# Optimization experiments

Hardware: AMD Instinct MI355X
Metric: run time of the kernel (lower is better)

## Reference

```python
import jax, jax.numpy as jnp
import numpy as np

B, SQ, SK, D_MODEL, H, D = 2, 2048, 2048, 1024, 16, 64


def setup_inputs() -> dict:
    key = jax.random.key(0)
    ks = jax.random.split(key, 10)
    s = 1.0 / np.sqrt(D_MODEL)
    return {
        "x": jax.random.normal(ks[0], (B, SK, D_MODEL), jnp.float32),
        "x2": jax.random.normal(ks[1], (B, SQ, D_MODEL), jnp.float32),
        "Wq": jax.random.normal(ks[2], (H, D_MODEL, D), jnp.float32) * s,
        "bq": jax.random.normal(ks[3], (H, D), jnp.float32) * s,
        "Wk": jax.random.normal(ks[4], (H, D_MODEL, D), jnp.float32) * s,
        "bk": jax.random.normal(ks[5], (H, D), jnp.float32) * s,
        "Wv": jax.random.normal(ks[6], (H, D_MODEL, D), jnp.float32) * s,
        "bv": jax.random.normal(ks[7], (H, D), jnp.float32) * s,
        "Wo": jax.random.normal(ks[8], (D_MODEL, D_MODEL), jnp.float32) * s,
        "bo": jax.random.normal(ks[9], (D_MODEL,), jnp.float32) * s,
    }


def reference(x, x2, Wq, bq, Wk, bk, Wv, bv, Wo, bo):
    # Batched per-head projections (fuses the Python per-head loop).
    # q: [B, H, SQ, D]; k,v: [B, H, SK, D]
    q = jnp.einsum("bsm,hmd->bhsd", x2, Wq) + bq[None, :, None, :]
    k = jnp.einsum("bsm,hmd->bhsd", x, Wk) + bk[None, :, None, :]
    v = jnp.einsum("bsm,hmd->bhsd", x, Wv) + bv[None, :, None, :]
    scale = 1.0 / jnp.sqrt(jnp.asarray(D, q.dtype))
    scores = jnp.einsum("bhqd,bhkd->bhqk", q, k) * scale  # [B,H,SQ,SK]
    attn = jax.nn.softmax(scores, axis=-1)
    o = jnp.einsum("bhqk,bhkd->bhqd", attn, v)  # [B,H,SQ,D]
    # concat heads along feature dim (head-major order matches torch.cat)
    o = o.transpose(0, 2, 1, 3).reshape(B, SQ, H * D)
    # final projection; dropout is identity in eval mode
    return o @ Wo.T + bo
```

## Files before the change

### kernel.cpp

```cpp
#include <hip/hip_runtime.h>
#include <math.h>

#define B_   2
#define SQ_  2048
#define SK_  2048
#define DM_  1024
#define H_   16
#define D_   64

typedef __attribute__((ext_vector_type(8))) short bf16x8;
typedef __attribute__((ext_vector_type(4))) float f32x4;
typedef unsigned int u32;

__device__ __forceinline__ short f2bf(float f) {
    union { float f; unsigned u; } v; v.f = f;
    unsigned r = v.u + 0x7FFFu + ((v.u >> 16) & 1u);
    return (short)(r >> 16);
}
__device__ __forceinline__ u32 pk2bf(float x, float y) {
    union { float f; u32 u; } a, b; a.f = x; b.f = y;
    return ((a.u + 0x8000u) >> 16) | ((b.u + 0x8000u) & 0xFFFF0000u);
}
__device__ __forceinline__ u32 pkbf_rh(float x, float y) {
    union { float f; u32 u; } a, b; a.f = x; b.f = y;
    return __builtin_amdgcn_perm(b.u + 0x8000u, a.u + 0x8000u, 0x07060302u);
}

__device__ __forceinline__ void gll16(const void* g, void* l) {
    __builtin_amdgcn_global_load_lds(
        (const __attribute__((address_space(1))) u32*)g,
        (__attribute__((address_space(3))) u32*)l, 16, 0, 0);
}

__global__ __launch_bounds__(256) void prep_kernel(
    const float* __restrict__ Wq, const float* __restrict__ Wk,
    const float* __restrict__ Wv, const float* __restrict__ Wo,
    const float* __restrict__ x,  const float* __restrict__ x2,
    short* __restrict__ WqT, short* __restrict__ WkT,
    short* __restrict__ WvT, short* __restrict__ Wob,
    short* __restrict__ xb,  short* __restrict__ x2b)
{
    const int t = threadIdx.x;
    const int z = blockIdx.z;
    if (z >= 3) {
        const float* src = (z == 3) ? Wo : (z == 4) ? x : x2;
        short* dst       = (z == 3) ? Wob : (z == 4) ? xb : x2b;
        int nloop = (z == 3) ? 4 : 16;
        int bid = blockIdx.y * 16 + blockIdx.x;
        #pragma unroll 4
        for (int j = 0; j < nloop; j++) {
            int i = bid * (nloop * 256) + j * 256 + t;
            float4 v = ((const float4*)src)[i];
            short4 s;
            s.x = f2bf(v.x); s.y = f2bf(v.y); s.z = f2bf(v.z); s.w = f2bf(v.w);
            ((short4*)dst)[i] = s;
        }
        return;
    }
    const float* W = (z == 0) ? Wq : (z == 1) ? Wk : Wv;
    short* WT      = (z == 0) ? WqT : (z == 1) ? WkT : WvT;
    const int h  = blockIdx.y;
    const int m0 = blockIdx.x * 64;
    __shared__ short Ls[64][68];

    #pragma unroll
    for (int it = 0; it < 4; it++) {
        int lin = it * 256 + t;
        int m = lin >> 4, d4 = lin & 15;
        float4 v = *(const float4*)&W[((long)h * DM_ + m0 + m) * D_ + d4 * 4];
        short4 s;
        s.x = f2bf(v.x); s.y = f2bf(v.y); s.z = f2bf(v.z); s.w = f2bf(v.w);
        *(short4*)&Ls[m][d4 * 4] = s;
    }
    __syncthreads();
    #pragma unroll
    for (int it = 0; it < 2; it++) {
        int d = (t >> 3) + it * 32, scol = t & 7;
        bf16x8 vv;
        #pragma unroll
        for (int j = 0; j < 8; j++) vv[j] = Ls[scol * 8 + j][d];
        *(bf16x8*)&WT[((long)h * 64 + d) * DM_ + m0 + scol * 8] = vv;
    }
}

template <int MODE>
__device__ __forceinline__ void gemm_core(
    const short* __restrict__ A, const short* __restrict__ Bw,
    const float* __restrict__ bias, void* __restrict__ outp,
    int r0, int n0, float oscale)
{
    __shared__ short As[128 * 64];
    __shared__ short Bs[128 * 64];

    const int t    = threadIdx.x;
    const int w    = t >> 6;
    const int ln   = t & 63;
    const int l15  = ln & 15;
    const int quad = ln >> 4;
    const int wr   = w >> 1;
    const int wc   = w & 1;

    f32x4 acc[4][4];
    #pragma unroll
    for (int i = 0; i < 4; i++)
        #pragma unroll
        for (int j = 0; j < 4; j++) acc[i][j] = (f32x4){0.f, 0.f, 0.f, 0.f};

    const int srow = ln >> 3;
    const int sc   = (ln & 7) ^ srow;
    const int rsw  = l15 & 7;

    for (int k0 = 0; k0 < 1024; k0 += 64) {
        __syncthreads();
        #pragma unroll
        for (int j = 0; j < 4; j++) {
            int q   = w * 4 + j;
            int row = q * 8 + srow;
            gll16(A  + ((long)(r0 + row) << 10) + k0 + sc * 8, As + q * 512);
            gll16(Bw + ((long)(n0 + row) << 10) + k0 + sc * 8, Bs + q * 512);
        }
        __syncthreads();
        #pragma unroll
        for (int kh = 0; kh < 2; kh++) {
            bf16x8 af[4], bfr[4];
            #pragma unroll
            for (int i = 0; i < 4; i++) {
                int ra = wr * 64 + i * 16 + l15;
                int rb = wc * 64 + i * 16 + l15;
                int pc = ((kh * 4 + quad) ^ rsw) * 8;
                af[i]  = *(const bf16x8*)&As[ra * 64 + pc];
                bfr[i] = *(const bf16x8*)&Bs[rb * 64 + pc];
            }
            #pragma unroll
            for (int i = 0; i < 4; i++)
                #pragma unroll
                for (int j = 0; j < 4; j++)
                    acc[i][j] = __builtin_amdgcn_mfma_f32_16x16x32_bf16(
                        af[i], bfr[j], acc[i][j], 0, 0, 0);
        }
    }

    #pragma unroll
    for (int j = 0; j < 4; j++) {
        int col = n0 + wc * 64 + j * 16 + l15;
        float bv = bias[col];
        if (MODE == 2) {
            int hh = col >> 6, dd = col & 63;
            #pragma unroll
            for (int i = 0; i < 4; i++) {
                int rowb = r0 + wr * 64 + i * 16 + quad * 4;
                int bb = rowb >> 11, ss = rowb & 2047;
                int sl = ss & 63;
                int sp = (ss & ~63) | (sl & 35) | ((sl & 12) << 1) | ((sl & 16) >> 2);
                short4 sv;
                sv.x = f2bf(acc[i][j][0] + bv);
                sv.y = f2bf(acc[i][j][1] + bv);
                sv.z = f2bf(acc[i][j][2] + bv);
                sv.w = f2bf(acc[i][j][3] + bv);
                *(short4*)&((short*)outp)[
                    ((long)(((bb << 4) + hh) * 64 + dd) << 11) + sp] = sv;
            }
        } else {
            #pragma unroll
            for (int i = 0; i < 4; i++) {
                int rowb = r0 + wr * 64 + i * 16 + quad * 4;
                #pragma unroll
                for (int r = 0; r < 4; r++) {
                    float v = (acc[i][j][r] + bv) * oscale;
                    if (MODE == 0)
                        ((short*)outp)[(long)(rowb + r) * 1024 + col] = f2bf(v);
                    else
                        ((float*)outp)[(long)(rowb + r) * 1024 + col] = v;
                }
            }
        }
    }
}

#define QSCALE 0.180336880977f

__global__ __launch_bounds__(256) void gemm_qkv_kernel(
    const short* __restrict__ x2b, const short* __restrict__ xb,
    const short* __restrict__ WqT, const short* __restrict__ WkT,
    const short* __restrict__ WvT,
    const float* __restrict__ bq, const float* __restrict__ bk,
    const float* __restrict__ bv,
    short* __restrict__ Qb, short* __restrict__ Kb, short* __restrict__ VT)
{
    const int z = blockIdx.z;
    if (z == 0) {
        gemm_core<0>(x2b, WqT, bq, Qb, blockIdx.x * 128, blockIdx.y * 128, QSCALE);
    } else if (z == 1) {
        gemm_core<0>(xb, WkT, bk, Kb, blockIdx.x * 128, blockIdx.y * 128, 1.0f);
    } else {
        gemm_core<2>(xb, WvT, bv, VT, blockIdx.x * 128, blockIdx.y * 128, 1.0f);
    }
}

__global__ __launch_bounds__(256) void gemm_out_kernel(
    const short* __restrict__ A, const short* __restrict__ Bw,
    const float* __restrict__ bias, float* __restrict__ outp)
{
    __shared__ short As[64 * 64];
    __shared__ short Bs[128 * 64];

    const int r0   = blockIdx.x * 64;
    const int n0   = blockIdx.y * 128;
    const int t    = threadIdx.x;
    const int w    = t >> 6;
    const int ln   = t & 63;
    const int l15  = ln & 15;
    const int quad = ln >> 4;
    const int wr   = w >> 1;
    const int wc   = w & 1;

    f32x4 acc[2][4];
    #pragma unroll
    for (int i = 0; i < 2; i++)
        #pragma unroll
        for (int j = 0; j < 4; j++) acc[i][j] = (f32x4){0.f, 0.f, 0.f, 0.f};

    const int srow = ln >> 3;
    const int sc   = (ln & 7) ^ srow;
    const int rsw  = l15 & 7;

    for (int k0 = 0; k0 < 1024; k0 += 64) {
        __syncthreads();
        #pragma unroll
        for (int j = 0; j < 6; j++) {
            int q = w * 6 + j;
            if (q < 8) {
                int row = q * 8 + srow;
                gll16(A + ((long)(r0 + row) << 10) + k0 + sc * 8, As + q * 512);
            } else {
                int qb = q - 8;
                int row = qb * 8 + srow;
                gll16(Bw + ((long)(n0 + row) << 10) + k0 + sc * 8, Bs + qb * 512);
            }
        }
        __syncthreads();
        #pragma unroll
        for (int kh = 0; kh < 2; kh++) {
            int pc = ((kh * 4 + quad) ^ rsw) * 8;
            bf16x8 af[2], bfr[4];
            #pragma unroll
            for (int i = 0; i < 2; i++)
                af[i] = *(const bf16x8*)&As[(wr * 32 + i * 16 + l15) * 64 + pc];
            #pragma unroll
            for (int j = 0; j < 4; j++)
                bfr[j] = *(const bf16x8*)&Bs[(wc * 64 + j * 16 + l15) * 64 + pc];
            #pragma unroll
            for (int i = 0; i < 2; i++)
                #pragma unroll
                for (int j = 0; j < 4; j++)
                    acc[i][j] = __builtin_amdgcn_mfma_f32_16x16x32_bf16(
                        af[i], bfr[j], acc[i][j], 0, 0, 0);
        }
    }

    #pragma unroll
    for (int j = 0; j < 4; j++) {
        int col = n0 + wc * 64 + j * 16 + l15;
        float bv = bias[col];
        #pragma unroll
        for (int i = 0; i < 2; i++) {
            int rowb = r0 + wr * 32 + i * 16 + quad * 4;
            #pragma unroll
            for (int r = 0; r < 4; r++)
                outp[(long)(rowb + r) * 1024 + col] = acc[i][j][r] + bv;
        }
    }
}

__global__ __launch_bounds__(256, 2) void flash_kernel(
    const short* __restrict__ Q, const short* __restrict__ K,
    const short* __restrict__ VT, short* __restrict__ O)
{
    const int t    = threadIdx.x;
    const int wave = t >> 6;
    const int ln   = t & 63;
    const int l15  = ln & 15;
    const int quad = ln >> 4;
    const int bh = blockIdx.y;
    const int b  = bh >> 4;
    const int h  = bh & 15;
    const int q0 = blockIdx.x * 128;
    const int wq = q0 + wave * 32;

    __shared__ short Ks[2][2][64 * 64];
    __shared__ short Vs[2][2][64 * 64];

    const int srow = ln >> 3;
    const int sc   = (ln & 7) ^ srow;
    const int rsw  = l15 & 7;
    const int pc0  = ((quad    ) ^ rsw) * 8;
    const int pc1  = ((quad + 4) ^ rsw) * 8;
    const int rb   = l15 * 64;

    bf16x8 aQ0[2], aQ1[2];
    #pragma unroll
    for (int qg = 0; qg < 2; qg++) {
        const short* Qp = Q + ((long)(b * SQ_ + wq + qg * 16 + l15)) * 1024
                            + h * 64 + quad * 8;
        aQ0[qg] = *(const bf16x8*)(Qp);
        aQ1[qg] = *(const bf16x8*)(Qp + 32);
    }

    bf16x8 ones;
    #pragma unroll
    for (int j = 0; j < 8; j++) ones[j] = (short)0x3F80;

    const f32x4 fz = (f32x4){0.f, 0.f, 0.f, 0.f};

    f32x4 o_acc[2][4];
    f32x4 l_acc[2];
    #pragma unroll
    for (int qg = 0; qg < 2; qg++) {
        l_acc[qg] = fz;
        #pragma unroll
        for (int i = 0; i < 4; i++) o_acc[qg][i] = fz;
    }

    const short* Kbase = K  + ((long)b * SK_) * 1024 + h * 64;
    const short* Vbase = VT + (long)bh * D_ * SK_;
    const int qqa = wave * 2, qqb = wave * 2 + 1;
    const int rowa = qqa * 8 + srow, rowb_ = qqb * 8 + srow;

    #define STAGE(bufp, half, kbase)                                            \
        gll16(Kbase + (long)((kbase) + rowa)  * 1024 + sc * 8,                  \
              &Ks[bufp][half][qqa * 512]);                                      \
        gll16(Kbase + (long)((kbase) + rowb_) * 1024 + sc * 8,                  \
              &Ks[bufp][half][qqb * 512]);                                      \
        gll16(Vbase + (long)rowa  * 2048 + (kbase) + sc * 8,                    \
              &Vs[bufp][half][qqa * 512]);                                      \
        gll16(Vbase + (long)rowb_ * 2048 + (kbase) + sc * 8,                    \
              &Vs[bufp][half][qqb * 512]);

    STAGE(0, 0, 0)
    STAGE(0, 1, 64)

    int cur = 0;
    for (int k0 = 0; k0 < SK_; k0 += 128) {
        __syncthreads();
        if (k0 + 128 < SK_) {
            int nx = cur ^ 1;
            STAGE(nx, 0, k0 + 128)
            STAGE(nx, 1, k0 + 192)
        }
        const short* K0 = &Ks[cur][0][0];
        const short* K1 = &Ks[cur][1][0];
        const short* V0 = &Vs[cur][0][0];
        const short* V1 = &Vs[cur][1][0];

        bf16x8 kfA[8];
        #pragma unroll
        for (int kt = 0; kt < 4; kt++) {
            const short* kr = &K0[kt * 1024 + rb];
            kfA[kt * 2    ] = *(const bf16x8*)&kr[pc0];
            kfA[kt * 2 + 1] = *(const bf16x8*)&kr[pc1];
        }

        bf16x8 kfB[8];
        #pragma unroll
        for (int kt = 0; kt < 4; kt++) {
            const short* kr = &K1[kt * 1024 + rb];
            kfB[kt * 2    ] = *(const bf16x8*)&kr[pc0];
            kfB[kt * 2 + 1] = *(const bf16x8*)&kr[pc1];
        }
        f32x4 zA[2][4], zB[2][4];
        #pragma unroll
        for (int kt = 0; kt < 4; kt++)
            #pragma unroll
            for (int qg = 0; qg < 2; qg++) {
                f32x4 z = __builtin_amdgcn_mfma_f32_16x16x32_bf16(kfA[kt * 2], aQ0[qg], fz, 0, 0, 0);
                zA[qg][kt] = __builtin_amdgcn_mfma_f32_16x16x32_bf16(kfA[kt * 2 + 1], aQ1[qg], z, 0, 0, 0);
            }

        bf16x8 vfA[8];
        #pragma unroll
        for (int dt = 0; dt < 4; dt++) {
            const short* vr = &V0[dt * 1024 + rb];
            vfA[dt * 2    ] = *(const bf16x8*)&vr[pc0];
            vfA[dt * 2 + 1] = *(const bf16x8*)&vr[pc1];
        }
        u32 pwA[2][8], pwB[2][8];
        #pragma unroll
        for (int kt = 0; kt < 4; kt++) {
            #pragma unroll
            for (int qg = 0; qg < 2; qg++) {
                f32x4 z = __builtin_amdgcn_mfma_f32_16x16x32_bf16(kfB[kt * 2], aQ0[qg], fz, 0, 0, 0);
                zB[qg][kt] = __builtin_amdgcn_mfma_f32_16x16x32_bf16(kfB[kt * 2 + 1], aQ1[qg], z, 0, 0, 0);
            }
            #pragma unroll
            for (int qg = 0; qg < 2; qg++) {
                f32x4 s = zA[qg][kt];
                pwA[qg][kt * 2    ] = pkbf_rh(__builtin_amdgcn_exp2f(s[0]),
                                              __builtin_amdgcn_exp2f(s[1]));
                pwA[qg][kt * 2 + 1] = pkbf_rh(__builtin_amdgcn_exp2f(s[2]),
                                              __builtin_amdgcn_exp2f(s[3]));
            }
        }

        bf16x8 aP0A[2], aP1A[2];
        #pragma unroll
        for (int qg = 0; qg < 2; qg++) {
            union { bf16x8 v; u32 w[4]; } u0, u1;
            u0.w[0] = pwA[qg][0]; u0.w[1] = pwA[qg][1];
            u0.w[2] = pwA[qg][2]; u0.w[3] = pwA[qg][3];
            u1.w[0] = pwA[qg][4]; u1.w[1] = pwA[qg][5];
            u1.w[2] = pwA[qg][6]; u1.w[3] = pwA[qg][7];
            aP0A[qg] = u0.v; aP1A[qg] = u1.v;
            l_acc[qg] = __builtin_amdgcn_mfma_f32_16x16x32_bf16(aP0A[qg], ones, l_acc[qg], 0, 0, 0);
            l_acc[qg] = __builtin_amdgcn_mfma_f32_16x16x32_bf16(aP1A[qg], ones, l_acc[qg], 0, 0, 0);
        }

        bf16x8 vfB[8];
        #pragma unroll
        for (int dt = 0; dt < 4; dt++) {
            const short* vr = &V1[dt * 1024 + rb];
            vfB[dt * 2    ] = *(const bf16x8*)&vr[pc0];
            vfB[dt * 2 + 1] = *(const bf16x8*)&vr[pc1];
        }
        #pragma unroll
        for (int dt = 0; dt < 4; dt++) {
            #pragma unroll
            for (int qg = 0; qg < 2; qg++) {
                o_acc[qg][dt] = __builtin_amdgcn_mfma_f32_16x16x32_bf16(aP0A[qg], vfA[dt * 2    ], o_acc[qg][dt], 0, 0, 0);
                o_acc[qg][dt] = __builtin_amdgcn_mfma_f32_16x16x32_bf16(aP1A[qg], vfA[dt * 2 + 1], o_acc[qg][dt], 0, 0, 0);
            }
            #pragma unroll
            for (int qg = 0; qg < 2; qg++) {
                f32x4 s = zB[qg][dt];
                pwB[qg][dt * 2    ] = pkbf_rh(__builtin_amdgcn_exp2f(s[0]),
                                              __builtin_amdgcn_exp2f(s[1]));
                pwB[qg][dt * 2 + 1] = pkbf_rh(__builtin_amdgcn_exp2f(s[2]),
                                              __builtin_amdgcn_exp2f(s[3]));
            }
        }

        bf16x8 aP0B[2], aP1B[2];
        #pragma unroll
        for (int qg = 0; qg < 2; qg++) {
            union { bf16x8 v; u32 w[4]; } u0, u1;
            u0.w[0] = pwB[qg][0]; u0.w[1] = pwB[qg][1];
            u0.w[2] = pwB[qg][2]; u0.w[3] = pwB[qg][3];
            u1.w[0] = pwB[qg][4]; u1.w[1] = pwB[qg][5];
            u1.w[2] = pwB[qg][6]; u1.w[3] = pwB[qg][7];
            aP0B[qg] = u0.v; aP1B[qg] = u1.v;
        }
        __builtin_amdgcn_s_setprio(1);
        #pragma unroll
        for (int qg = 0; qg < 2; qg++) {
            l_acc[qg] = __builtin_amdgcn_mfma_f32_16x16x32_bf16(aP0B[qg], ones, l_acc[qg], 0, 0, 0);
            l_acc[qg] = __builtin_amdgcn_mfma_f32_16x16x32_bf16(aP1B[qg], ones, l_acc[qg], 0, 0, 0);
        }
        #pragma unroll
        for (int dt = 0; dt < 4; dt++) {
            #pragma unroll
            for (int qg = 0; qg < 2; qg++) {
                o_acc[qg][dt] = __builtin_amdgcn_mfma_f32_16x16x32_bf16(aP0B[qg], vfB[dt * 2    ], o_acc[qg][dt], 0, 0, 0);
                o_acc[qg][dt] = __builtin_amdgcn_mfma_f32_16x16x32_bf16(aP1B[qg], vfB[dt * 2 + 1], o_acc[qg][dt], 0, 0, 0);
            }
        }
        __builtin_amdgcn_s_setprio(0);
        cur ^= 1;
    }
    #undef STAGE

    #pragma unroll
    for (int qg = 0; qg < 2; qg++) {
        #pragma unroll
        for (int r = 0; r < 4; r++) {
            float inv = 1.0f / l_acc[qg][r];
            long row = (long)b * SQ_ + wq + qg * 16 + quad * 4 + r;
            short* Op = O + row * 1024 + h * 64 + l15;
            #pragma unroll
            for (int dt = 0; dt < 4; dt++)
                Op[dt * 16] = f2bf(o_acc[qg][dt][r] * inv);
        }
    }
}

extern "C" void kernel_launch(void* const* d_in, const int* in_sizes, int n_in,
                              void* d_out, int out_size, void* d_ws, size_t ws_size,
                              hipStream_t stream) {
    const float* x  = (const float*)d_in[0];
    const float* x2 = (const float*)d_in[1];
    const float* Wq = (const float*)d_in[2];
    const float* bq = (const float*)d_in[3];
    const float* Wk = (const float*)d_in[4];
    const float* bk = (const float*)d_in[5];
    const float* Wv = (const float*)d_in[6];
    const float* bv = (const float*)d_in[7];
    const float* Wo = (const float*)d_in[8];
    const float* bo = (const float*)d_in[9];
    float* out = (float*)d_out;

    const size_t nAct = (size_t)B_ * SK_ * DM_;
    const size_t nW   = (size_t)DM_ * DM_;
    short* bufA = (short*)d_ws;
    short* bufB = bufA + nAct;
    short* Qb   = bufB + nAct;
    short* Kb   = Qb + nAct;
    short* VTws = Kb + nAct;
    short* WqT  = VTws + nAct;
    short* WkT  = WqT + nW;
    short* WvT  = WkT + nW;
    short* Wob  = WvT + nW;

    prep_kernel<<<dim3(16, 16, 6), 256, 0, stream>>>(
        Wq, Wk, Wv, Wo, x, x2, WqT, WkT, WvT, Wob, bufA, bufB);

    gemm_qkv_kernel<<<dim3(32, 8, 3), 256, 0, stream>>>(
        bufB, bufA, WqT, WkT, WvT, bq, bk, bv, Qb, Kb, VTws);

    flash_kernel<<<dim3(16, 32), 256, 0, stream>>>(Qb, Kb, VTws, bufB);
    gemm_out_kernel<<<dim3(64, 8), 256, 0, stream>>>(bufB, Wob, bo, out);
}
```

Measured before the change: 204.6 us.

## Double-buffer LDS tiles in QKV and output projection GEMMs

Both projection GEMMs now use two LDS buffers. Each iteration issues the async global-to-LDS loads for the next K slice before running the MFMAs on the current slice, and drops one barrier per iteration. The aim is to overlap global memory latency with matrix compute. The cost is doubled LDS use (64 KB per block in the QKV kernel), which may lower the number of resident blocks per CU.

```diff
diff --git a/kernel.cpp b/kernel.cpp
--- a/kernel.cpp
+++ b/kernel.cpp
@@ -83,15 +83,27 @@
     }
 }
 
+__device__ __forceinline__ void gemm_stage(
+    short* __restrict__ Asb, short* __restrict__ Bsb,
+    const short* __restrict__ A, const short* __restrict__ Bw,
+    int r0, int n0, int k0c, int w, int srow, int sc)
+{
+    #pragma unroll
+    for (int j = 0; j < 4; j++) {
+        int q   = w * 4 + j;
+        int row = q * 8 + srow;
+        gll16(A  + ((long)(r0 + row) << 10) + k0c + sc * 8, Asb + q * 512);
+        gll16(Bw + ((long)(n0 + row) << 10) + k0c + sc * 8, Bsb + q * 512);
+    }
+}
+
 template <int MODE>
 __device__ __forceinline__ void gemm_core(
+    short* __restrict__ Ls,
     const short* __restrict__ A, const short* __restrict__ Bw,
     const float* __restrict__ bias, void* __restrict__ outp,
     int r0, int n0, float oscale)
 {
-    __shared__ short As[128 * 64];
-    __shared__ short Bs[128 * 64];
-
     const int t    = threadIdx.x;
     const int w    = t >> 6;
     const int ln   = t & 63;
@@ -110,16 +122,17 @@
     const int sc   = (ln & 7) ^ srow;
     const int rsw  = l15 & 7;
 
+    gemm_stage(Ls, Ls + 8192, A, Bw, r0, n0, 0, w, srow, sc);
+
+    int cur = 0;
     for (int k0 = 0; k0 < 1024; k0 += 64) {
         __syncthreads();
-        #pragma unroll
-        for (int j = 0; j < 4; j++) {
-            int q   = w * 4 + j;
-            int row = q * 8 + srow;
-            gll16(A  + ((long)(r0 + row) << 10) + k0 + sc * 8, As + q * 512);
-            gll16(Bw + ((long)(n0 + row) << 10) + k0 + sc * 8, Bs + q * 512);
-        }
-        __syncthreads();
+        if (k0 + 64 < 1024) {
+            short* Anx = Ls + (cur ^ 1) * 16384;
+            gemm_stage(Anx, Anx + 8192, A, Bw, r0, n0, k0 + 64, w, srow, sc);
+        }
+        const short* Asb = Ls + cur * 16384;
+        const short* Bsb = Asb + 8192;
         #pragma unroll
         for (int kh = 0; kh < 2; kh++) {
             bf16x8 af[4], bfr[4];
@@ -128,8 +141,8 @@
                 int ra = wr * 64 + i * 16 + l15;
                 int rb = wc * 64 + i * 16 + l15;
                 int pc = ((kh * 4 + quad) ^ rsw) * 8;
-                af[i]  = *(const bf16x8*)&As[ra * 64 + pc];
-                bfr[i] = *(const bf16x8*)&Bs[rb * 64 + pc];
+                af[i]  = *(const bf16x8*)&Asb[ra * 64 + pc];
+                bfr[i] = *(const bf16x8*)&Bsb[rb * 64 + pc];
             }
             #pragma unroll
             for (int i = 0; i < 4; i++)
@@ -138,6 +151,7 @@
                     acc[i][j] = __builtin_amdgcn_mfma_f32_16x16x32_bf16(
                         af[i], bfr[j], acc[i][j], 0, 0, 0);
         }
+        cur ^= 1;
     }
 
     #pragma unroll
@@ -187,13 +201,33 @@
     const float* __restrict__ bv,
     short* __restrict__ Qb, short* __restrict__ Kb, short* __restrict__ VT)
 {
+    __shared__ short Ls[2 * 16384];
     const int z = blockIdx.z;
     if (z == 0) {
-        gemm_core<0>(x2b, WqT, bq, Qb, blockIdx.x * 128, blockIdx.y * 128, QSCALE);
+        gemm_core<0>(Ls, x2b, WqT, bq, Qb, blockIdx.x * 128, blockIdx.y * 128, QSCALE);
     } else if (z == 1) {
-        gemm_core<0>(xb, WkT, bk, Kb, blockIdx.x * 128, blockIdx.y * 128, 1.0f);
+        gemm_core<0>(Ls, xb, WkT, bk, Kb, blockIdx.x * 128, blockIdx.y * 128, 1.0f);
     } else {
-        gemm_core<2>(xb, WvT, bv, VT, blockIdx.x * 128, blockIdx.y * 128, 1.0f);
+        gemm_core<2>(Ls, xb, WvT, bv, VT, blockIdx.x * 128, blockIdx.y * 128, 1.0f);
+    }
+}
+
+__device__ __forceinline__ void gout_stage(
+    short* __restrict__ Asb, short* __restrict__ Bsb,
+    const short* __restrict__ A, const short* __restrict__ Bw,
+    int r0, int n0, int k0c, int w, int srow, int sc)
+{
+    #pragma unroll
+    for (int j = 0; j < 6; j++) {
+        int q = w * 6 + j;
+        if (q < 8) {
+            int row = q * 8 + srow;
+            gll16(A + ((long)(r0 + row) << 10) + k0c + sc * 8, Asb + q * 512);
+        } else {
+            int qb = q - 8;
+            int row = qb * 8 + srow;
+            gll16(Bw + ((long)(n0 + row) << 10) + k0c + sc * 8, Bsb + qb * 512);
+        }
     }
 }
 
@@ -201,8 +235,7 @@
     const short* __restrict__ A, const short* __restrict__ Bw,
     const float* __restrict__ bias, float* __restrict__ outp)
 {
-    __shared__ short As[64 * 64];
-    __shared__ short Bs[128 * 64];
+    __shared__ short Ls[2 * 12288];
 
     const int r0   = blockIdx.x * 64;
     const int n0   = blockIdx.y * 128;
@@ -224,31 +257,27 @@
     const int sc   = (ln & 7) ^ srow;
     const int rsw  = l15 & 7;
 
+    gout_stage(Ls, Ls + 4096, A, Bw, r0, n0, 0, w, srow, sc);
+
+    int cur = 0;
     for (int k0 = 0; k0 < 1024; k0 += 64) {
         __syncthreads();
-        #pragma unroll
-        for (int j = 0; j < 6; j++) {
-            int q = w * 6 + j;
-            if (q < 8) {
-                int row = q * 8 + srow;
-                gll16(A + ((long)(r0 + row) << 10) + k0 + sc * 8, As + q * 512);
-            } else {
-                int qb = q - 8;
-                int row = qb * 8 + srow;
-                gll16(Bw + ((long)(n0 + row) << 10) + k0 + sc * 8, Bs + qb * 512);
-            }
-        }
-        __syncthreads();
+        if (k0 + 64 < 1024) {
+            short* Anx = Ls + (cur ^ 1) * 12288;
+            gout_stage(Anx, Anx + 4096, A, Bw, r0, n0, k0 + 64, w, srow, sc);
+        }
+        const short* Asb = Ls + cur * 12288;
+        const short* Bsb = Asb + 4096;
         #pragma unroll
         for (int kh = 0; kh < 2; kh++) {
             int pc = ((kh * 4 + quad) ^ rsw) * 8;
             bf16x8 af[2], bfr[4];
             #pragma unroll
             for (int i = 0; i < 2; i++)
-                af[i] = *(const bf16x8*)&As[(wr * 32 + i * 16 + l15) * 64 + pc];
+                af[i] = *(const bf16x8*)&Asb[(wr * 32 + i * 16 + l15) * 64 + pc];
             #pragma unroll
             for (int j = 0; j < 4; j++)
-                bfr[j] = *(const bf16x8*)&Bs[(wc * 64 + j * 16 + l15) * 64 + pc];
+                bfr[j] = *(const bf16x8*)&Bsb[(wc * 64 + j * 16 + l15) * 64 + pc];
             #pragma unroll
             for (int i = 0; i < 2; i++)
                 #pragma unroll
@@ -256,6 +285,7 @@
                     acc[i][j] = __builtin_amdgcn_mfma_f32_16x16x32_bf16(
                         af[i], bfr[j], acc[i][j], 0, 0, 0);
         }
+        cur ^= 1;
     }
 
     #pragma unroll
```

Measured after the change: 198.2 us. 3.2% less time.
